# Performance work log

Measured on AMD Instinct MI355X. Metric: run time of the kernel, lower is better.

## Reference

```python
import jax, jax.numpy as jnp
import numpy as np

N = 8192      # neurons per layer (and n_inputs)
L = 16        # hidden topological layers
DEG = 128     # avg in-degree
E = N * DEG   # edges per hidden layer
NOUT = 16     # output neurons
EOUT = N * NOUT  # edges into output layer


def _lrelu(v):
    return jnp.where(v >= 0, v, 0.01 * v)


def setup_inputs() -> dict:
    key = jax.random.key(0)
    ks = jax.random.split(key, 7)
    x = jax.random.normal(ks[0], (N,), dtype=jnp.float32)
    edge_src = jax.random.randint(ks[1], (L, E), 0, N, dtype=jnp.int32)
    edge_dst = jax.random.randint(ks[2], (L, E), 0, N, dtype=jnp.int32)
    # scale weights ~1/sqrt(degree) so 16 layers of accumulation stay finite
    edge_w = jax.random.normal(ks[3], (L, E), dtype=jnp.float32) / np.float32(np.sqrt(DEG))
    out_src = jax.random.randint(ks[4], (EOUT,), 0, N, dtype=jnp.int32)
    out_dst = jax.random.randint(ks[5], (EOUT,), 0, NOUT, dtype=jnp.int32)
    out_w = jax.random.normal(ks[6], (EOUT,), dtype=jnp.float32) / np.float32(np.sqrt(EOUT / NOUT))
    return {"x": x, "edge_w": edge_w, "out_w": out_w,
            "edge_src": edge_src, "edge_dst": edge_dst,
            "out_src": out_src, "out_dst": out_dst}


def reference(x, edge_w, out_w, edge_src, edge_dst, out_src, out_dst):
    n = x.shape[0]

    def step(vals, layer):
        src, dst, w = layer
        # per-node weighted accumulation: n.value += i.value * i.weight[n]
        new = jax.ops.segment_sum(vals[src] * w, dst, num_segments=n)
        return _lrelu(new), None  # leaky_relu on every non-INPUT node

    vals, _ = jax.lax.scan(step, x, (edge_src, edge_dst, edge_w))
    o = jax.ops.segment_sum(vals[out_src] * out_w, out_dst, num_segments=NOUT)
    o = _lrelu(o)
    return jax.nn.softmax(o, axis=0)
```

## Files before the change

### kernel.cpp

```cpp
#include <hip/hip_runtime.h>

#define NN    8192
#define NL    16
#define NE    (NN * 128)
#define NOUTC 16
#define EOUTC (NN * NOUTC)

#define NBLK  256
#define NTHR  512
#define EPB   (NE / NBLK)

__device__ __forceinline__ float lrelu(float v) { return v >= 0.f ? v : 0.01f * v; }

__global__ __launch_bounds__(NTHR) void scatter_kernel(
    const float* __restrict__ sv,
    const int*   __restrict__ es,
    const int*   __restrict__ ed,
    const float* __restrict__ ew,
    float*       __restrict__ partials)
{
    __shared__ float vals[NN];
    __shared__ float accs[NN];
    const int tid = threadIdx.x;
    const int b   = blockIdx.x;

    for (int i = tid * 4; i < NN; i += NTHR * 4) {
        *(float4*)(vals + i) = *(const float4*)(sv + i);
        *(float4*)(accs + i) = make_float4(0.f, 0.f, 0.f, 0.f);
    }
    __syncthreads();

    const int base = b * EPB;
    #pragma unroll
    for (int it = 0; it < EPB / (NTHR * 4); ++it) {
        const int e = base + it * NTHR * 4 + tid * 4;
        int4   s = *(const int4*)(es + e);
        int4   d = *(const int4*)(ed + e);
        float4 w = *(const float4*)(ew + e);
        atomicAdd(&accs[d.x], vals[s.x] * w.x);
        atomicAdd(&accs[d.y], vals[s.y] * w.y);
        atomicAdd(&accs[d.z], vals[s.z] * w.z);
        atomicAdd(&accs[d.w], vals[s.w] * w.w);
    }
    __syncthreads();

    float* prow = partials + (size_t)b * NN;
    for (int i = tid * 4; i < NN; i += NTHR * 4)
        *(float4*)(prow + i) = *(const float4*)(accs + i);
}

__global__ __launch_bounds__(256) void reduce_kernel(
    const float* __restrict__ partials,
    float*       __restrict__ accv)
{
    __shared__ float sred[8][32];
    const int b  = blockIdx.x;
    const int nl = threadIdx.x & 31;
    const int kg = threadIdx.x >> 5;
    const int n  = b * 32 + nl;

    float s = 0.f;
    #pragma unroll
    for (int k = 0; k < NBLK / 8; ++k)
        s += partials[(size_t)(kg + k * 8) * NN + n];
    sred[kg][nl] = s;
    __syncthreads();
    if (threadIdx.x < 32) {
        float t = 0.f;
        #pragma unroll
        for (int j = 0; j < 8; ++j) t += sred[j][threadIdx.x];
        accv[b * 32 + threadIdx.x] = lrelu(t);
    }
}

__global__ __launch_bounds__(NTHR) void out_scatter_kernel(
    const float* __restrict__ accv,
    const int*   __restrict__ out_src,
    const int*   __restrict__ out_dst,
    const float* __restrict__ out_w,
    float*       __restrict__ outs)
{
    __shared__ float bins[NOUTC];
    const int tid = threadIdx.x;
    if (tid < NOUTC) bins[tid] = 0.f;
    __syncthreads();
    const int g = blockIdx.x * NTHR + tid;
    atomicAdd(&bins[out_dst[g]], accv[out_src[g]] * out_w[g]);
    __syncthreads();
    if (tid < NOUTC) outs[(size_t)blockIdx.x * NOUTC + tid] = bins[tid];
}

__global__ __launch_bounds__(256) void final_kernel(
    const float* __restrict__ outs, float* __restrict__ out)
{
    __shared__ float red[16][17];
    const int tid = threadIdx.x;
    const int j = tid & 15, g = tid >> 4;
    float s = 0.f;
    #pragma unroll
    for (int r = 0; r < NBLK / 16; ++r)
        s += outs[(size_t)(g + r * 16) * NOUTC + j];
    red[g][j] = s;
    __syncthreads();
    if (tid < NOUTC) {
        float t = 0.f;
        #pragma unroll
        for (int g2 = 0; g2 < 16; ++g2) t += red[g2][tid];
        float v = lrelu(t);
        float m = v;
        #pragma unroll
        for (int off = 8; off >= 1; off >>= 1)
            m = fmaxf(m, __shfl_xor(m, off, 64));
        float e = __expf(v - m);
        float ssum = e;
        #pragma unroll
        for (int off = 8; off >= 1; off >>= 1)
            ssum += __shfl_xor(ssum, off, 64);
        out[tid] = e / ssum;
    }
}

extern "C" void kernel_launch(void* const* d_in, const int* in_sizes, int n_in,
                              void* d_out, int out_size, void* d_ws, size_t ws_size,
                              hipStream_t stream) {
    const float* x        = (const float*)d_in[0];
    const float* edge_w   = (const float*)d_in[1];
    const float* out_w    = (const float*)d_in[2];
    const int*   edge_src = (const int*)d_in[3];
    const int*   edge_dst = (const int*)d_in[4];
    const int*   out_src  = (const int*)d_in[5];
    const int*   out_dst  = (const int*)d_in[6];

    float* partials = (float*)d_ws;
    float* accv     = partials + (size_t)NBLK * NN;
    float* outs     = accv + NN;
    float* out      = (float*)d_out;

    for (int l = 0; l < NL; ++l) {
        const float* sv = (l == 0) ? x : accv;
        scatter_kernel<<<NBLK, NTHR, 0, stream>>>(
            sv,
            edge_src + (size_t)l * NE,
            edge_dst + (size_t)l * NE,
            edge_w   + (size_t)l * NE,
            partials);
        reduce_kernel<<<NBLK, 256, 0, stream>>>(partials, accv);
    }

    out_scatter_kernel<<<NBLK, NTHR, 0, stream>>>(accv, out_src, out_dst, out_w, outs);
    final_kernel<<<1, 256, 0, stream>>>(outs, out);
}
```

Baseline: 401.6 us.

## Fuse all layers into one persistent cooperative kernel with grid barriers

Replaces the 34 separate kernel launches (a scatter and a reduce per layer, plus the output stages) with a single cooperative kernel. Blocks synchronise through a hierarchical atomic grid barrier in workspace memory, and shared-memory scatter, partial reduction, output scatter and softmax all run inside it. Block size doubles to 1024 so each thread handles one int4 of edges per layer. The goal is to remove per-launch overhead and inter-kernel gaps, at the cost of spin-barrier latency and relaxed atomic global loads.

```diff
diff --git a/kernel.cpp b/kernel.cpp
--- a/kernel.cpp
+++ b/kernel.cpp
@@ -7,116 +7,151 @@
 #define EOUTC (NN * NOUTC)
 
 #define NBLK  256
-#define NTHR  512
+#define NTHR  1024
 #define EPB   (NE / NBLK)
+
+#define AGENT __HIP_MEMORY_SCOPE_AGENT
 
 __device__ __forceinline__ float lrelu(float v) { return v >= 0.f ? v : 0.01f * v; }
 
-__global__ __launch_bounds__(NTHR) void scatter_kernel(
-    const float* __restrict__ sv,
-    const int*   __restrict__ es,
-    const int*   __restrict__ ed,
-    const float* __restrict__ ew,
-    float*       __restrict__ partials)
+__device__ __forceinline__ float gload(const float* p) {
+    return __hip_atomic_load(p, __ATOMIC_RELAXED, AGENT);
+}
+__device__ __forceinline__ void gstore(float* p, float v) {
+    __hip_atomic_store(p, v, __ATOMIC_RELAXED, AGENT);
+}
+
+__device__ __forceinline__ void gbarrier(int* bar, int b, int epoch) {
+    int old = __hip_atomic_fetch_add(&bar[(b & 15) * 16], 1, __ATOMIC_ACQ_REL, AGENT);
+    if (old == epoch * 16 - 1) {
+        int mo = __hip_atomic_fetch_add(&bar[256], 1, __ATOMIC_ACQ_REL, AGENT);
+        if (mo == epoch * 16 - 1) {
+            __hip_atomic_store(&bar[272], epoch, __ATOMIC_RELEASE, AGENT);
+        }
+    }
+    while (__hip_atomic_load(&bar[272], __ATOMIC_ACQUIRE, AGENT) < epoch) {
+        __builtin_amdgcn_s_sleep(1);
+    }
+}
+
+__global__ __launch_bounds__(512) void zero_bar_kernel(int* __restrict__ bar) {
+    if (threadIdx.x < 288) bar[threadIdx.x] = 0;
+}
+
+__global__ __launch_bounds__(NTHR) void nn_kernel(
+    const float* __restrict__ x,
+    const float* __restrict__ edge_w,
+    const int*   __restrict__ edge_src,
+    const int*   __restrict__ edge_dst,
+    const float* __restrict__ out_w,
+    const int*   __restrict__ out_src,
+    const int*   __restrict__ out_dst,
+    float* __restrict__ partials,
+    float* __restrict__ accv,
+    float* __restrict__ outs,
+    int*   __restrict__ bar,
+    float* __restrict__ out)
 {
     __shared__ float vals[NN];
     __shared__ float accs[NN];
+    __shared__ float bins[NOUTC];
+
     const int tid = threadIdx.x;
     const int b   = blockIdx.x;
+    int ep = 0;
 
-    for (int i = tid * 4; i < NN; i += NTHR * 4) {
-        *(float4*)(vals + i) = *(const float4*)(sv + i);
-        *(float4*)(accs + i) = make_float4(0.f, 0.f, 0.f, 0.f);
+    for (int l = 0; l < NL; ++l) {
+        if (l == 0) {
+            for (int i = tid * 4; i < NN; i += NTHR * 4)
+                *(float4*)(vals + i) = *(const float4*)(x + i);
+        } else {
+            for (int i = tid; i < NN; i += NTHR)
+                vals[i] = gload(accv + i);
+        }
+        for (int i = tid * 4; i < NN; i += NTHR * 4)
+            *(float4*)(accs + i) = make_float4(0.f, 0.f, 0.f, 0.f);
+        __syncthreads();
+
+        {
+            const size_t eb = (size_t)l * NE + (size_t)b * EPB + (size_t)tid * 4;
+            int4   s = *(const int4*)(edge_src + eb);
+            int4   d = *(const int4*)(edge_dst + eb);
+            float4 w = *(const float4*)(edge_w + eb);
+            atomicAdd(&accs[d.x], vals[s.x] * w.x);
+            atomicAdd(&accs[d.y], vals[s.y] * w.y);
+            atomicAdd(&accs[d.z], vals[s.z] * w.z);
+            atomicAdd(&accs[d.w], vals[s.w] * w.w);
+        }
+        __syncthreads();
+
+        for (int i = tid; i < NN; i += NTHR)
+            gstore(partials + (size_t)b * NN + i, accs[i]);
+        __syncthreads();
+        ++ep; if (tid == 0) gbarrier(bar, b, ep);
+        __syncthreads();
+
+        {
+            const int kg = tid >> 5;
+            const int nl = tid & 31;
+            const int n  = b * 32 + nl;
+            float s = 0.f;
+            #pragma unroll
+            for (int j = 0; j < 8; ++j)
+                s += gload(partials + (size_t)(kg + 32 * j) * NN + n);
+            float* sred = vals;
+            sred[kg * 33 + nl] = s;
+            __syncthreads();
+            if (tid < 32) {
+                float t = 0.f;
+                #pragma unroll
+                for (int r = 0; r < 32; ++r) t += sred[r * 33 + tid];
+                gstore(accv + b * 32 + tid, lrelu(t));
+            }
+        }
+        __syncthreads();
+        ++ep; if (tid == 0) gbarrier(bar, b, ep);
+        __syncthreads();
+    }
+
+    if (tid < NOUTC) bins[tid] = 0.f;
+    __syncthreads();
+    if (tid < 512) {
+        const int g = b * 512 + tid;
+        atomicAdd(&bins[out_dst[g]], gload(accv + out_src[g]) * out_w[g]);
     }
     __syncthreads();
-
-    const int base = b * EPB;
-    #pragma unroll
-    for (int it = 0; it < EPB / (NTHR * 4); ++it) {
-        const int e = base + it * NTHR * 4 + tid * 4;
-        int4   s = *(const int4*)(es + e);
-        int4   d = *(const int4*)(ed + e);
-        float4 w = *(const float4*)(ew + e);
-        atomicAdd(&accs[d.x], vals[s.x] * w.x);
-        atomicAdd(&accs[d.y], vals[s.y] * w.y);
-        atomicAdd(&accs[d.z], vals[s.z] * w.z);
-        atomicAdd(&accs[d.w], vals[s.w] * w.w);
-    }
+    if (tid < NOUTC) gstore(outs + (size_t)b * NOUTC + tid, bins[tid]);
+    __syncthreads();
+    ++ep; if (tid == 0) gbarrier(bar, b, ep);
     __syncthreads();
 
-    float* prow = partials + (size_t)b * NN;
-    for (int i = tid * 4; i < NN; i += NTHR * 4)
-        *(float4*)(prow + i) = *(const float4*)(accs + i);
-}
-
-__global__ __launch_bounds__(256) void reduce_kernel(
-    const float* __restrict__ partials,
-    float*       __restrict__ accv)
-{
-    __shared__ float sred[8][32];
-    const int b  = blockIdx.x;
-    const int nl = threadIdx.x & 31;
-    const int kg = threadIdx.x >> 5;
-    const int n  = b * 32 + nl;
-
-    float s = 0.f;
-    #pragma unroll
-    for (int k = 0; k < NBLK / 8; ++k)
-        s += partials[(size_t)(kg + k * 8) * NN + n];
-    sred[kg][nl] = s;
-    __syncthreads();
-    if (threadIdx.x < 32) {
-        float t = 0.f;
-        #pragma unroll
-        for (int j = 0; j < 8; ++j) t += sred[j][threadIdx.x];
-        accv[b * 32 + threadIdx.x] = lrelu(t);
-    }
-}
-
-__global__ __launch_bounds__(NTHR) void out_scatter_kernel(
-    const float* __restrict__ accv,
-    const int*   __restrict__ out_src,
-    const int*   __restrict__ out_dst,
-    const float* __restrict__ out_w,
-    float*       __restrict__ outs)
-{
-    __shared__ float bins[NOUTC];
-    const int tid = threadIdx.x;
-    if (tid < NOUTC) bins[tid] = 0.f;
-    __syncthreads();
-    const int g = blockIdx.x * NTHR + tid;
-    atomicAdd(&bins[out_dst[g]], accv[out_src[g]] * out_w[g]);
-    __syncthreads();
-    if (tid < NOUTC) outs[(size_t)blockIdx.x * NOUTC + tid] = bins[tid];
-}
-
-__global__ __launch_bounds__(256) void final_kernel(
-    const float* __restrict__ outs, float* __restrict__ out)
-{
-    __shared__ float red[16][17];
-    const int tid = threadIdx.x;
-    const int j = tid & 15, g = tid >> 4;
-    float s = 0.f;
-    #pragma unroll
-    for (int r = 0; r < NBLK / 16; ++r)
-        s += outs[(size_t)(g + r * 16) * NOUTC + j];
-    red[g][j] = s;
-    __syncthreads();
-    if (tid < NOUTC) {
-        float t = 0.f;
-        #pragma unroll
-        for (int g2 = 0; g2 < 16; ++g2) t += red[g2][tid];
-        float v = lrelu(t);
-        float m = v;
-        #pragma unroll
-        for (int off = 8; off >= 1; off >>= 1)
-            m = fmaxf(m, __shfl_xor(m, off, 64));
-        float e = __expf(v - m);
-        float ssum = e;
-        #pragma unroll
-        for (int off = 8; off >= 1; off >>= 1)
-            ssum += __shfl_xor(ssum, off, 64);
-        out[tid] = e / ssum;
+    if (b == 0) {
+        float* red = vals;
+        if (tid < 256) {
+            const int j = tid & 15, g = tid >> 4;
+            float s = 0.f;
+            #pragma unroll
+            for (int r = 0; r < 16; ++r)
+                s += gload(outs + (size_t)(g + r * 16) * NOUTC + j);
+            red[g * 17 + j] = s;
+        }
+        __syncthreads();
+        if (tid < NOUTC) {
+            float t = 0.f;
+            #pragma unroll
+            for (int g2 = 0; g2 < 16; ++g2) t += red[g2 * 17 + tid];
+            float v = lrelu(t);
+            float m = v;
+            #pragma unroll
+            for (int off = 8; off >= 1; off >>= 1)
+                m = fmaxf(m, __shfl_xor(m, off, 64));
+            float e = __expf(v - m);
+            float ssum = e;
+            #pragma unroll
+            for (int off = 8; off >= 1; off >>= 1)
+                ssum += __shfl_xor(ssum, off, 64);
+            out[tid] = e / ssum;
+        }
     }
 }
 
@@ -134,19 +169,17 @@
     float* partials = (float*)d_ws;
     float* accv     = partials + (size_t)NBLK * NN;
     float* outs     = accv + NN;
+    int*   bar      = (int*)(outs + NBLK * NOUTC);
     float* out      = (float*)d_out;
 
-    for (int l = 0; l < NL; ++l) {
-        const float* sv = (l == 0) ? x : accv;
-        scatter_kernel<<<NBLK, NTHR, 0, stream>>>(
-            sv,
-            edge_src + (size_t)l * NE,
-            edge_dst + (size_t)l * NE,
-            edge_w   + (size_t)l * NE,
-            partials);
-        reduce_kernel<<<NBLK, 256, 0, stream>>>(partials, accv);
-    }
+    zero_bar_kernel<<<1, 512, 0, stream>>>(bar);
 
-    out_scatter_kernel<<<NBLK, NTHR, 0, stream>>>(accv, out_src, out_dst, out_w, outs);
-    final_kernel<<<1, 256, 0, stream>>>(outs, out);
+    void* args[] = { (void*)&x, (void*)&edge_w, (void*)&edge_src, (void*)&edge_dst,
+                     (void*)&out_w, (void*)&out_src, (void*)&out_dst,
+                     (void*)&partials, (void*)&accv, (void*)&outs, (void*)&bar,
+                     (void*)&out };
+
+    hipLaunchCooperativeKernel((const void*)nn_kernel,
+                               dim3(NBLK), dim3(NTHR),
+                               args, 0, stream);
 }
```

Result: slower. 1.021 ms (+154.2%).
